# Kernel optimization log

Measured on AMD Instinct MI355X. Metric: run time of the kernel, lower is better.

## Reference

```python
import jax, jax.numpy as jnp
import numpy as np

NOISE_EPS = 1e-2   # Shazeer noisy-gating stddev floor
LN_EPS = 1e-6
LOSS_COEF = 0.01
K = 2              # num_activated_experts


def _layer_norm(x, w, b):
    mu = jnp.mean(x, axis=-1, keepdims=True)
    var = jnp.var(x, axis=-1, keepdims=True)
    return (x - mu) * jax.lax.rsqrt(var + LN_EPS) * w + b


def _cv_squared(v):
    return jnp.var(v) / (jnp.mean(v) ** 2 + 1e-10)


def _normal_cdf(z):
    return 0.5 * (1.0 + jax.scipy.special.erf(z / jnp.sqrt(jnp.asarray(2.0, z.dtype))))


def setup_inputs() -> dict:
    key = jax.random.key(0)
    ks = jax.random.split(key, 8)
    N, D, H, O, E = 8192, 512, 1024, 512, 8
    x = jax.random.normal(ks[0], (N, D), jnp.float32)
    x_offsets = jnp.sort(jax.random.randint(ks[1], (17,), 0, N)).astype(jnp.int64)
    noise = jax.random.normal(ks[2], (N, E), jnp.float32)
    s = 0.02
    return {
        "x": x,
        "x_offsets": x_offsets,
        "max_seq_len": 2048,
        "noise": noise,
        "norm_w": jnp.ones((D,), jnp.float32),
        "norm_bias": jnp.zeros((D,), jnp.float32),
        "w_gate": jax.random.normal(ks[3], (D, E), jnp.float32) * s,
        "w_noise": jax.random.normal(ks[4], (D, E), jnp.float32) * s,
        "W1": jax.random.normal(ks[5], (E, H, D), jnp.float32) * s,  # [E, model_d, input]
        "b1": jnp.zeros((E, H), jnp.float32),
        "W2": jax.random.normal(ks[6], (E, O, H), jnp.float32) * s,  # [E, output, model_d]
        "b2": jnp.zeros((E, O), jnp.float32),
        "output_weight": jax.random.normal(ks[7], (D, O), jnp.float32) * s,
    }


def reference(x, x_offsets, max_seq_len, noise, norm_w, norm_bias, w_gate, w_noise,
              W1, b1, W2, b2, output_weight):
    N, D = x.shape
    E = w_gate.shape[1]
    k_plus = min(K + 1, E)

    # pre-norm
    x_norm = _layer_norm(x, norm_w, norm_bias)

    # noisy top-k gating (training path)
    clean_logits = x_norm @ w_gate                      # [N, E]
    noise_stddev = jax.nn.softplus(x_norm @ w_noise) + NOISE_EPS
    noisy_logits = clean_logits + noise * noise_stddev

    top_logits, top_indices = jax.lax.top_k(noisy_logits, k_plus)   # [N, k+1]
    top_k_logits = top_logits[:, :K]
    top_k_indices = top_indices[:, :K]
    top_k_gates = jax.nn.softmax(top_k_logits, axis=-1)             # [N, K]

    rows = jnp.arange(N)[:, None]
    gates = jnp.zeros((N, E), top_k_gates.dtype).at[rows, top_k_indices].set(top_k_gates)

    # load = prob each expert is in top-k under the gating noise (Shazeer)
    flat = top_logits.reshape(-1)
    pos_in = jnp.arange(N) * k_plus + K
    thr_in = flat[pos_in][:, None]          # (k+1)-th value: threshold if already in
    thr_out = flat[pos_in - 1][:, None]     # k-th value: threshold if currently out
    is_in = noisy_logits > thr_in
    prob_in = _normal_cdf((clean_logits - thr_in) / noise_stddev)
    prob_out = _normal_cdf((clean_logits - thr_out) / noise_stddev)
    load_probs = jnp.where(is_in, prob_in, prob_out)                # [N, E]

    loss = LOSS_COEF * (_cv_squared(gates.sum(0)) + _cv_squared(load_probs.sum(0)))

    # dispatch stats: tokens per expert
    lengths = jnp.zeros((E,), jnp.float32).at[top_k_indices.reshape(-1)].add(1.0)
    load = lengths / lengths.sum()

    # grouped expert MLP (dense one-hot combine; gates are 0 for unrouted experts)
    h = jnp.einsum('nd,ehd->neh', x_norm, W1) + b1                  # [N, E, H]
    a = jax.nn.silu(h)
    y_e = jnp.einsum('neh,eoh->neo', a, W2) + b2                    # [N, E, O]
    y_moe = jnp.einsum('ne,neo->no', gates, y_e)                    # [N, O]

    # shared expert: addmm(y, shared_x=x, output_weight)
    y = y_moe + x @ output_weight
    return y, loss, load
```

## Files before the change

kernel.cpp:

```cpp
#include <hip/hip_runtime.h>
#include <math.h>

typedef unsigned short u16;
typedef unsigned int u32;

#define N_ROWS 8192
#define DDIM 512
#define HDIM 1024
#define ODIM 512
#define NEXP 8
#define MAXPAIRS (N_ROWS * 2)
#define MAXPOS (MAXPAIRS + NEXP * 128)
#define MAXTILES (MAXPOS / 128)

#define SM_CNT 0
#define SM_CUR 8
#define SM_AOFF 16
#define SM_GSUM 32
#define SM_LSUM 40
#define SM_WORDS 64

using short8 = __attribute__((ext_vector_type(8))) short;
using float4v = __attribute__((ext_vector_type(4))) float;

__device__ __forceinline__ u16 f2bf(float f) {
    union { float f; u32 u; } v; v.f = f;
    u32 u = v.u;
    return (u16)((u + 0x7fffu + ((u >> 16) & 1u)) >> 16);
}

__device__ __forceinline__ void async_copy16(u16* lds, const u16* g) {
    __builtin_amdgcn_global_load_lds(
        (const __attribute__((address_space(1))) void*)g,
        (__attribute__((address_space(3))) void*)lds, 16, 0, 0);
}

__global__ __launch_bounds__(512) void init1_kernel(int* small, float* zeropage) {
    int i = threadIdx.x;
    if (i < SM_WORDS) small[i] = 0;
    zeropage[i] = 0.f;
}

#define W1CONV_BLOCKS 4096
#define GATE_BLOCKS 512
#define OWT_BLOCKS 256
#define BUCKET_BLOCKS 68
#define W2CONV_BLOCKS 2048
__global__ __launch_bounds__(256) void combo_kernel(
    const float* __restrict__ x, const float* __restrict__ noise,
    const float* __restrict__ norm_w, const float* __restrict__ norm_b,
    const float* __restrict__ w_gate, const float* __restrict__ w_noise,
    const float* __restrict__ W1, const float* __restrict__ ow,
    const float* __restrict__ W2,
    u16* __restrict__ xnorm_bf, u16* __restrict__ x_bf,
    int* __restrict__ pair_expert, float* __restrict__ pair_gate,
    u16* __restrict__ W1b, u16* __restrict__ owT, u16* __restrict__ W2b,
    int* __restrict__ small, int* __restrict__ bucket_rows)
{
    __shared__ __align__(16) float sh[NEXP * DDIM * 2 + 64];
    int b = blockIdx.x, tid = threadIdx.x;

    if (b >= GATE_BLOCKS) {
        int cb = b - GATE_BLOCKS;
        if (cb < W1CONV_BLOCKS) {
            size_t i = (size_t)cb * 256 + tid;
            float4 v = ((const float4*)W1)[i];
            ushort4 o;
            o.x = f2bf(v.x); o.y = f2bf(v.y); o.z = f2bf(v.z); o.w = f2bf(v.w);
            ((ushort4*)W1b)[i] = o;
        } else if (cb < W1CONV_BLOCKS + OWT_BLOCKS) {
            float (*tile)[33] = (float(*)[33])sh;
            int t = cb - W1CONV_BLOCKS;
            int bx = (t & 15) * 32, by = (t >> 4) * 32;
            int tx = tid & 31, ty = tid >> 5;
            for (int r = ty; r < 32; r += 8) tile[r][tx] = ow[(size_t)(by + r) * ODIM + bx + tx];
            __syncthreads();
            for (int r = ty; r < 32; r += 8) owT[(size_t)(bx + r) * DDIM + by + tx] = f2bf(tile[tx][r]);
        } else if (cb < W1CONV_BLOCKS + OWT_BLOCKS + BUCKET_BLOCKS) {
            int i = (cb - W1CONV_BLOCKS - OWT_BLOCKS) * 256 + tid;
            if (i < MAXPOS) bucket_rows[i] = -1;
        } else {
            int j = cb - W1CONV_BLOCKS - OWT_BLOCKS - BUCKET_BLOCKS;
            size_t i = (size_t)j * 512 + tid;
#pragma unroll
            for (int t = 0; t < 2; t++, i += 256) {
                float4 v = ((const float4*)W2)[i];
                ushort4 o;
                o.x = f2bf(v.x); o.y = f2bf(v.y); o.z = f2bf(v.z); o.w = f2bf(v.w);
                ((ushort4*)W2b)[i] = o;
            }
        }
        return;
    }

    float* wgT = sh;
    float* wnT = sh + NEXP * DDIM;
    float* blk_g = sh + 2 * NEXP * DDIM;
    float* blk_l = blk_g + NEXP;
    int* blk_c = (int*)(blk_l + NEXP);
    float* smf = (float*)small;

    for (int i = tid; i < NEXP * DDIM; i += 256) {
        int d = i >> 3, e = i & 7;
        wgT[e * DDIM + d] = w_gate[i];
        wnT[e * DDIM + d] = w_noise[i];
    }
    if (tid < NEXP) { blk_g[tid] = 0.f; blk_l[tid] = 0.f; blk_c[tid] = 0; }
    __syncthreads();

    int wave = tid >> 6, lane = tid & 63;
    float nw[8], nb[8];
#pragma unroll
    for (int j = 0; j < 8; j++) { nw[j] = norm_w[j * 64 + lane]; nb[j] = norm_b[j * 64 + lane]; }

    for (int r = 0; r < 4; ++r) {
        int row = b * 16 + wave * 4 + r;
        const float* xr = x + (size_t)row * DDIM;
        float xv[8], s = 0.f, s2 = 0.f;
#pragma unroll
        for (int j = 0; j < 8; j++) { float v = xr[j * 64 + lane]; xv[j] = v; s += v; s2 += v * v; }
#pragma unroll
        for (int o = 32; o; o >>= 1) { s += __shfl_xor(s, o, 64); s2 += __shfl_xor(s2, o, 64); }
        float mu = s * (1.f / DDIM);
        float var = s2 * (1.f / DDIM) - mu * mu;
        float rstd = rsqrtf(var + 1e-6f);

        float acc[16];
#pragma unroll
        for (int e = 0; e < 16; e++) acc[e] = 0.f;
#pragma unroll
        for (int j = 0; j < 8; j++) {
            float v = (xv[j] - mu) * rstd * nw[j] + nb[j];
            int d = j * 64 + lane;
            xnorm_bf[(size_t)row * DDIM + d] = f2bf(v);
            x_bf[(size_t)row * DDIM + d] = f2bf(xv[j]);
#pragma unroll
            for (int e = 0; e < 8; e++) {
                acc[e] += v * wgT[e * DDIM + d];
                acc[8 + e] += v * wnT[e * DDIM + d];
            }
        }
#pragma unroll
        for (int e = 0; e < 16; e++)
#pragma unroll
            for (int o = 32; o; o >>= 1) acc[e] += __shfl_xor(acc[e], o, 64);

        float cl[8], sd[8], nz[8];
#pragma unroll
        for (int e = 0; e < 8; e++) {
            cl[e] = acc[e];
            float t = acc[8 + e];
            float sp = fmaxf(t, 0.f) + log1pf(expf(-fabsf(t)));
            sd[e] = sp + 0.01f;
            nz[e] = cl[e] + noise[(size_t)row * NEXP + e] * sd[e];
        }
        int idx[3]; float val[3]; u32 msk = 0;
#pragma unroll
        for (int t = 0; t < 3; t++) {
            float best = -INFINITY; int bi = 0;
#pragma unroll
            for (int e = 0; e < 8; e++)
                if (!((msk >> e) & 1) && nz[e] > best) { best = nz[e]; bi = e; }
            idx[t] = bi; val[t] = best; msk |= 1u << bi;
        }
        float e1 = expf(val[1] - val[0]);
        float g0 = 1.f / (1.f + e1), g1 = e1 / (1.f + e1);
        float thr_in = val[2], thr_out = val[1];

        if (lane == 0) {
            pair_expert[row * 2] = idx[0]; pair_gate[row * 2] = g0;
            pair_expert[row * 2 + 1] = idx[1]; pair_gate[row * 2 + 1] = g1;
            atomicAdd(&blk_g[idx[0]], g0); atomicAdd(&blk_g[idx[1]], g1);
            atomicAdd(&blk_c[idx[0]], 1); atomicAdd(&blk_c[idx[1]], 1);
#pragma unroll
            for (int e = 0; e < 8; e++) {
                float thr = (nz[e] > thr_in) ? thr_in : thr_out;
                float z = (cl[e] - thr) / sd[e];
                float p = 0.5f * (1.f + erff(z * 0.70710678118654752f));
                atomicAdd(&blk_l[e], p);
            }
        }
    }
    __syncthreads();
    if (tid < NEXP) {
        atomicAdd(smf + SM_GSUM + tid, blk_g[tid]);
        atomicAdd(smf + SM_LSUM + tid, blk_l[tid]);
        atomicAdd(&small[SM_CNT + tid], blk_c[tid]);
    }
}

__global__ __launch_bounds__(256) void scatter_kernel(
    const int* __restrict__ pair_expert, const float* __restrict__ pair_gate,
    int* __restrict__ small, int* __restrict__ bucket_rows, float* __restrict__ gate_by_pos,
    float* __restrict__ out_loss, float* __restrict__ out_load)
{
    __shared__ int aoff[NEXP + 1];
    __shared__ int blk_cnt[NEXP];
    __shared__ int blk_base[NEXP];
    int tid = threadIdx.x;
    if (tid == 0) {
        int acc = 0; aoff[0] = 0;
        for (int e = 0; e < NEXP; e++) { acc += (small[SM_CNT + e] + 127) & ~127; aoff[e + 1] = acc; }
    }
    if (tid < NEXP) blk_cnt[tid] = 0;
    __syncthreads();
    int p = blockIdx.x * 256 + tid;
    int e = pair_expert[p];
    int local = atomicAdd(&blk_cnt[e], 1);
    __syncthreads();
    if (tid < NEXP)
        blk_base[tid] = aoff[tid] + atomicAdd(&small[SM_CUR + tid], blk_cnt[tid]);
    if (blockIdx.x == 0 && tid < NEXP + 1) small[SM_AOFF + tid] = aoff[tid];
    __syncthreads();
    int pos = blk_base[e] + local;
    bucket_rows[pos] = p >> 1;
    gate_by_pos[pos] = pair_gate[p];

    if (blockIdx.x == 0 && tid == 0) {
        const float* gs = (const float*)small + SM_GSUM;
        const float* ls = (const float*)small + SM_LSUM;
        float cv[2];
        for (int t = 0; t < 2; t++) {
            const float* v = t ? ls : gs;
            float m = 0.f;
            for (int k = 0; k < NEXP; k++) m += v[k];
            m *= (1.f / NEXP);
            float var = 0.f;
            for (int k = 0; k < NEXP; k++) { float d = v[k] - m; var += d * d; }
            var *= (1.f / NEXP);
            cv[t] = var / (m * m + 1e-10f);
        }
        out_loss[0] = 0.01f * (cv[0] + cv[1]);
        int tot = 0;
        for (int k = 0; k < NEXP; k++) tot += small[SM_CNT + k];
        float inv = 1.f / (float)tot;
        for (int k = 0; k < NEXP; k++) out_load[k] = (float)small[SM_CNT + k] * inv;
    }
}

__global__ __launch_bounds__(256) void gemmA_kernel(
    const u16* __restrict__ xnorm, const u16* __restrict__ W1b,
    const u16* __restrict__ xbf, const u16* __restrict__ owT,
    const int* __restrict__ bucket_rows, const int* __restrict__ small,
    const float* __restrict__ b1, const u16* __restrict__ zeropage,
    u16* __restrict__ a_buf, float* __restrict__ y)
{
    constexpr int KD = 512;
    __shared__ __align__(16) u16 As[128 * 64];
    __shared__ __align__(16) u16 Bs[128 * 64];

    int tid = threadIdx.x;
    if (blockIdx.y >= 8) {
        int j = (blockIdx.y - 8) * 136 + blockIdx.x;
        if (j >= 256) return;
        int base = (j >> 2) * 128, bn = (j & 3) * 128;
        int wave = tid >> 6, lane = tid & 63;
        const int lrow = lane >> 2;
        const int kcol = (((lane & 3) ^ ((lane >> 3) & 3)) * 8);
        const int trow = wave * 32 + lrow;
        int wm = (wave & 1) * 64, wn = (wave >> 1) * 64;
        int fr = lane & 15, kq = lane >> 4;
        const int kg = ((kq ^ ((fr >> 1) & 3)) * 8);
        const u16* ga0 = xbf + (size_t)(base + trow) * KD + kcol;
        const u16* ga1 = xbf + (size_t)(base + trow + 16) * KD + kcol;
        const u16* gb0 = owT + (size_t)(bn + trow) * KD + kcol;
        const u16* gb1 = owT + (size_t)(bn + trow + 16) * KD + kcol;
        u16* As2 = (u16*)As; u16* Bs2 = (u16*)Bs;
        const int ofA0 = (wave * 32) * 32, ofA1 = (wave * 32 + 16) * 32;

        float4v acc[4][4];
#pragma unroll
        for (int i = 0; i < 4; i++)
#pragma unroll
            for (int jj = 0; jj < 4; jj++) acc[i][jj] = (float4v){0.f, 0.f, 0.f, 0.f};

        async_copy16(As2 + ofA0, ga0); async_copy16(As2 + ofA1, ga1);
        async_copy16(Bs2 + ofA0, gb0); async_copy16(Bs2 + ofA1, gb1);
        __syncthreads();
        int cur = 0;
        for (int t = 0; t < 16; ++t) {
            int nxt = cur ^ 1;
            if (t + 1 < 16) {
                int k1 = (t + 1) << 5;
                async_copy16(As2 + nxt * 4096 + ofA0, ga0 + k1);
                async_copy16(As2 + nxt * 4096 + ofA1, ga1 + k1);
                async_copy16(Bs2 + nxt * 4096 + ofA0, gb0 + k1);
                async_copy16(Bs2 + nxt * 4096 + ofA1, gb1 + k1);
            }
            short8 af[4], bf[4];
#pragma unroll
            for (int mt = 0; mt < 4; mt++) af[mt] = *(const short8*)&As2[cur * 4096 + (wm + mt * 16 + fr) * 32 + kg];
#pragma unroll
            for (int nt = 0; nt < 4; nt++) bf[nt] = *(const short8*)&Bs2[cur * 4096 + (wn + nt * 16 + fr) * 32 + kg];
#pragma unroll
            for (int mt = 0; mt < 4; mt++)
#pragma unroll
                for (int nt = 0; nt < 4; nt++)
                    acc[mt][nt] = __builtin_amdgcn_mfma_f32_16x16x32_bf16(af[mt], bf[nt], acc[mt][nt], 0, 0, 0);
            __syncthreads();
            cur = nxt;
        }
        int rbase = (lane >> 4) * 4, c16 = lane & 15;
#pragma unroll
        for (int mt = 0; mt < 4; mt++) {
            int gm = base + wm + mt * 16 + rbase;
#pragma unroll
            for (int nt = 0; nt < 4; nt++) {
                int gn = bn + wn + nt * 16 + c16;
#pragma unroll
                for (int r = 0; r < 4; r++)
                    y[(size_t)(gm + r) * ODIM + gn] = acc[mt][nt][r];
            }
        }
        return;
    }

    int base = blockIdx.x * 128;
    if (base >= small[SM_AOFF + 8]) return;
    int e = 0;
    while (e < 7 && base >= small[SM_AOFF + e + 1]) ++e;
    int bn = blockIdx.y * 128;
    const u16* Bsel = W1b + (size_t)e * HDIM * KD;

    int wave = tid >> 6, lane = tid & 63;
    int lr = lane >> 3;
    int lc = ((lane & 7) ^ lr) * 8;

    const u16* ga[4]; const u16* gb[4];
    u16* la[4]; u16* lb[4];
#pragma unroll
    for (int c = 0; c < 4; c++) {
        int tr = wave * 32 + c * 8;
        int r0 = bucket_rows[base + tr + lr];
        ga[c] = ((r0 < 0) ? zeropage : xnorm + (size_t)r0 * KD) + lc;
        gb[c] = Bsel + (size_t)(bn + tr + lr) * KD + lc;
        la[c] = &As[tr * 64];
        lb[c] = &Bs[tr * 64];
    }

    int wm = (wave & 1) * 64, wn = (wave >> 1) * 64;
    int fr = lane & 15, kq = lane >> 4, f7 = fr & 7;

    float4v acc[4][4];
#pragma unroll
    for (int i = 0; i < 4; i++)
#pragma unroll
        for (int j = 0; j < 4; j++) acc[i][j] = (float4v){0.f, 0.f, 0.f, 0.f};

    for (int k0 = 0; k0 < KD; k0 += 64) {
        __syncthreads();
#pragma unroll
        for (int c = 0; c < 4; c++) async_copy16(la[c], ga[c] + k0);
#pragma unroll
        for (int c = 0; c < 4; c++) async_copy16(lb[c], gb[c] + k0);
        __syncthreads();
        short8 af[4][2], bf[4][2];
#pragma unroll
        for (int mt = 0; mt < 4; mt++)
#pragma unroll
            for (int kh = 0; kh < 2; kh++)
                af[mt][kh] = *(const short8*)&As[(wm + mt * 16 + fr) * 64 + (((kq + 4 * kh) ^ f7) * 8)];
#pragma unroll
        for (int nt = 0; nt < 4; nt++)
#pragma unroll
            for (int kh = 0; kh < 2; kh++)
                bf[nt][kh] = *(const short8*)&Bs[(wn + nt * 16 + fr) * 64 + (((kq + 4 * kh) ^ f7) * 8)];
#pragma unroll
        for (int mt = 0; mt < 4; mt++)
#pragma unroll
            for (int nt = 0; nt < 4; nt++) {
                acc[mt][nt] = __builtin_amdgcn_mfma_f32_16x16x32_bf16(af[mt][0], bf[nt][0], acc[mt][nt], 0, 0, 0);
                acc[mt][nt] = __builtin_amdgcn_mfma_f32_16x16x32_bf16(af[mt][1], bf[nt][1], acc[mt][nt], 0, 0, 0);
            }
    }

    int rbase = (lane >> 4) * 4, c16 = lane & 15;
#pragma unroll
    for (int nt = 0; nt < 4; nt++) {
        int gn = bn + wn + nt * 16 + c16;
        float bv = b1[e * HDIM + gn];
#pragma unroll
        for (int mt = 0; mt < 4; mt++) {
            int gm = base + wm + mt * 16 + rbase;
#pragma unroll
            for (int r = 0; r < 4; r++) {
                float h = acc[mt][nt][r] + bv;
                float a = h * __builtin_amdgcn_rcpf(1.f + __expf(-h));
                a_buf[(size_t)(gm + r) * HDIM + gn] = f2bf(a);
            }
        }
    }
}

__global__ __launch_bounds__(512) void gemmB_kernel(
    const u16* __restrict__ a_buf, const u16* __restrict__ W2b,
    const int* __restrict__ bucket_rows, const int* __restrict__ small,
    const float* __restrict__ b2, const float* __restrict__ gate_by_pos,
    float* __restrict__ y)
{
    constexpr int KD = 1024;
    __shared__ __align__(16) u16 As[2][128 * 32];
    __shared__ __align__(16) u16 Bs[2][256 * 32];

    int tid = threadIdx.x;
    int wave = tid >> 6, lane = tid & 63;
    const int lrow = lane >> 2;
    const int kcol = (((lane & 3) ^ ((lane >> 3) & 3)) * 8);
    int wm = (wave >> 2) * 64, wn = (wave & 3) * 64;
    int fr = lane & 15, kq = lane >> 4;
    const int kg = ((kq ^ ((fr >> 1) & 3)) * 8);

    int base = blockIdx.x * 128;
    if (base >= small[SM_AOFF + 8]) return;
    int e = 0;
    while (e < 7 && base >= small[SM_AOFF + e + 1]) ++e;
    int bn = blockIdx.y * 256;

    const u16* ga0 = a_buf + (size_t)(base + wave * 16 + lrow) * KD + kcol;
    const u16* Bsel = W2b + (size_t)e * ODIM * KD;
    const u16* gb0 = Bsel + (size_t)(bn + wave * 32 + lrow) * KD + kcol;
    const u16* gb1 = Bsel + (size_t)(bn + wave * 32 + 16 + lrow) * KD + kcol;
    const int ofA = (wave * 16) * 32;
    const int ofB0 = (wave * 32) * 32;
    const int ofB1 = (wave * 32 + 16) * 32;

    float4v acc[4][4];
#pragma unroll
    for (int i = 0; i < 4; i++)
#pragma unroll
        for (int j = 0; j < 4; j++) acc[i][j] = (float4v){0.f, 0.f, 0.f, 0.f};

    constexpr int nk = KD >> 5;
    async_copy16(&As[0][ofA], ga0);
    async_copy16(&Bs[0][ofB0], gb0);
    async_copy16(&Bs[0][ofB1], gb1);
    __syncthreads();

    int cur = 0;
    for (int t = 0; t < nk; ++t) {
        int nxt = cur ^ 1;
        if (t + 1 < nk) {
            int k1 = (t + 1) << 5;
            async_copy16(&As[nxt][ofA], ga0 + k1);
            async_copy16(&Bs[nxt][ofB0], gb0 + k1);
            async_copy16(&Bs[nxt][ofB1], gb1 + k1);
        }
        short8 af[4], bf[4];
#pragma unroll
        for (int mt = 0; mt < 4; mt++) af[mt] = *(const short8*)&As[cur][(wm + mt * 16 + fr) * 32 + kg];
#pragma unroll
        for (int nt = 0; nt < 4; nt++) bf[nt] = *(const short8*)&Bs[cur][(wn + nt * 16 + fr) * 32 + kg];
#pragma unroll
        for (int mt = 0; mt < 4; mt++)
#pragma unroll
            for (int nt = 0; nt < 4; nt++)
                acc[mt][nt] = __builtin_amdgcn_mfma_f32_16x16x32_bf16(af[mt], bf[nt], acc[mt][nt], 0, 0, 0);
        __syncthreads();
        cur = nxt;
    }

    int rbase = (lane >> 4) * 4, c16 = lane & 15;
#pragma unroll
    for (int mt = 0; mt < 4; mt++) {
        int pos0 = base + wm + mt * 16 + rbase;
        int rows[4]; float gs[4];
#pragma unroll
        for (int r = 0; r < 4; r++) { rows[r] = bucket_rows[pos0 + r]; gs[r] = gate_by_pos[pos0 + r]; }
#pragma unroll
        for (int nt = 0; nt < 4; nt++) {
            int gn = bn + wn + nt * 16 + c16;
            float b2v = b2[e * ODIM + gn];
#pragma unroll
            for (int r = 0; r < 4; r++) {
                if (rows[r] >= 0)
                    unsafeAtomicAdd(&y[(size_t)rows[r] * ODIM + gn], gs[r] * (acc[mt][nt][r] + b2v));
            }
        }
    }
}

extern "C" void kernel_launch(void* const* d_in, const int* in_sizes, int n_in,
                              void* d_out, int out_size, void* d_ws, size_t ws_size,
                              hipStream_t stream)
{
    (void)in_sizes; (void)n_in; (void)out_size; (void)ws_size;
    const float* x = (const float*)d_in[0];
    const float* noise = (const float*)d_in[3];
    const float* norm_w = (const float*)d_in[4];
    const float* norm_b = (const float*)d_in[5];
    const float* w_gate = (const float*)d_in[6];
    const float* w_noise = (const float*)d_in[7];
    const float* W1 = (const float*)d_in[8];
    const float* b1 = (const float*)d_in[9];
    const float* W2 = (const float*)d_in[10];
    const float* b2 = (const float*)d_in[11];
    const float* ow = (const float*)d_in[12];

    float* y = (float*)d_out;
    float* out_loss = y + (size_t)N_ROWS * ODIM;
    float* out_load = out_loss + 1;

    char* ws = (char*)d_ws;
    size_t off = 0;
    auto alloc = [&](size_t b) { size_t p = off; off = (off + b + 255) & ~(size_t)255; return p; };
    u16* xnorm_bf = (u16*)(ws + alloc((size_t)N_ROWS * DDIM * 2));
    u16* x_bf     = (u16*)(ws + alloc((size_t)N_ROWS * DDIM * 2));
    u16* W1b      = (u16*)(ws + alloc((size_t)NEXP * HDIM * DDIM * 2));
    u16* W2b      = (u16*)(ws + alloc((size_t)NEXP * ODIM * HDIM * 2));
    u16* owT      = (u16*)(ws + alloc((size_t)DDIM * ODIM * 2));
    u16* a_buf    = (u16*)(ws + alloc((size_t)MAXPOS * HDIM * 2));
    int* pair_expert = (int*)(ws + alloc((size_t)MAXPAIRS * 4));
    float* pair_gate = (float*)(ws + alloc((size_t)MAXPAIRS * 4));
    float* gate_by_pos = (float*)(ws + alloc((size_t)MAXPOS * 4));
    int* bucket_rows = (int*)(ws + alloc((size_t)MAXPOS * 4));
    int* small       = (int*)(ws + alloc(SM_WORDS * 4));
    float* zeropage  = (float*)(ws + alloc(2048));

    init1_kernel<<<1, 512, 0, stream>>>(small, zeropage);
    combo_kernel<<<GATE_BLOCKS + W1CONV_BLOCKS + OWT_BLOCKS + BUCKET_BLOCKS + W2CONV_BLOCKS,
                   256, 0, stream>>>(
        x, noise, norm_w, norm_b, w_gate, w_noise, W1, ow, W2,
        xnorm_bf, x_bf, pair_expert, pair_gate, W1b, owT, W2b, small, bucket_rows);
    scatter_kernel<<<MAXPAIRS / 256, 256, 0, stream>>>(pair_expert, pair_gate, small,
                                                       bucket_rows, gate_by_pos, out_loss, out_load);
    gemmA_kernel<<<dim3(MAXTILES, 8 + 2), 256, 0, stream>>>(xnorm_bf, W1b,
                                                            x_bf, owT, bucket_rows, small, b1,
                                                            (const u16*)zeropage, a_buf, y);
    gemmB_kernel<<<dim3(MAXTILES, 2), 512, 0, stream>>>(a_buf, W2b, bucket_rows,
                                                        small, b2, gate_by_pos, y);
}
```

Before: 250.8 us.

## Replace atomic scatter-add in expert GEMM epilogue with buffered combine kernel

The second expert GEMM now writes gated per-position outputs to a dense fp32 buffer instead of atomically adding into y. A new combine kernel reads each token's two routed positions, found through a row-to-position map recorded during scatter, and adds them to the shared-expert result in y. This is meant to remove contended float atomics to global memory, at the cost of an extra kernel launch and roughly 34 MB of extra fp32 writes and reads.

```diff
diff --git a/kernel.cpp b/kernel.cpp
--- a/kernel.cpp
+++ b/kernel.cpp
@@ -192,6 +192,7 @@
 __global__ __launch_bounds__(256) void scatter_kernel(
     const int* __restrict__ pair_expert, const float* __restrict__ pair_gate,
     int* __restrict__ small, int* __restrict__ bucket_rows, float* __restrict__ gate_by_pos,
+    int* __restrict__ rowpos,
     float* __restrict__ out_loss, float* __restrict__ out_load)
 {
     __shared__ int aoff[NEXP + 1];
@@ -215,6 +216,7 @@
     int pos = blk_base[e] + local;
     bucket_rows[pos] = p >> 1;
     gate_by_pos[pos] = pair_gate[p];
+    rowpos[p] = pos;
 
     if (blockIdx.x == 0 && tid == 0) {
         const float* gs = (const float*)small + SM_GSUM;
@@ -396,7 +398,7 @@
     const u16* __restrict__ a_buf, const u16* __restrict__ W2b,
     const int* __restrict__ bucket_rows, const int* __restrict__ small,
     const float* __restrict__ b2, const float* __restrict__ gate_by_pos,
-    float* __restrict__ y)
+    float* __restrict__ ye)
 {
     constexpr int KD = 1024;
     __shared__ __align__(16) u16 As[2][128 * 32];
@@ -473,9 +475,29 @@
 #pragma unroll
             for (int r = 0; r < 4; r++) {
                 if (rows[r] >= 0)
-                    unsafeAtomicAdd(&y[(size_t)rows[r] * ODIM + gn], gs[r] * (acc[mt][nt][r] + b2v));
-            }
-        }
+                    ye[(size_t)(pos0 + r) * ODIM + gn] = gs[r] * (acc[mt][nt][r] + b2v);
+            }
+        }
+    }
+}
+
+__global__ __launch_bounds__(256) void combine_kernel(
+    const float* __restrict__ ye, const int* __restrict__ rowpos,
+    float* __restrict__ y)
+{
+    int tid = threadIdx.x;
+    int row = blockIdx.x * 16 + (tid >> 4);
+    int c0 = (tid & 15) * 32;
+    int p0 = rowpos[row * 2];
+    int p1 = rowpos[row * 2 + 1];
+    const float4* e0 = (const float4*)(ye + (size_t)p0 * ODIM + c0);
+    const float4* e1 = (const float4*)(ye + (size_t)p1 * ODIM + c0);
+    float4* yp = (float4*)(y + (size_t)row * ODIM + c0);
+#pragma unroll
+    for (int i = 0; i < 8; i++) {
+        float4 a = yp[i], b = e0[i], c = e1[i];
+        a.x += b.x + c.x; a.y += b.y + c.y; a.z += b.z + c.z; a.w += b.w + c.w;
+        yp[i] = a;
     }
 }
 
@@ -509,10 +531,12 @@
     u16* W2b      = (u16*)(ws + alloc((size_t)NEXP * ODIM * HDIM * 2));
     u16* owT      = (u16*)(ws + alloc((size_t)DDIM * ODIM * 2));
     u16* a_buf    = (u16*)(ws + alloc((size_t)MAXPOS * HDIM * 2));
+    float* ye     = (float*)(ws + alloc((size_t)MAXPOS * ODIM * 4));
     int* pair_expert = (int*)(ws + alloc((size_t)MAXPAIRS * 4));
     float* pair_gate = (float*)(ws + alloc((size_t)MAXPAIRS * 4));
     float* gate_by_pos = (float*)(ws + alloc((size_t)MAXPOS * 4));
     int* bucket_rows = (int*)(ws + alloc((size_t)MAXPOS * 4));
+    int* rowpos      = (int*)(ws + alloc((size_t)MAXPAIRS * 4));
     int* small       = (int*)(ws + alloc(SM_WORDS * 4));
     float* zeropage  = (float*)(ws + alloc(2048));
 
@@ -522,10 +546,12 @@
         x, noise, norm_w, norm_b, w_gate, w_noise, W1, ow, W2,
         xnorm_bf, x_bf, pair_expert, pair_gate, W1b, owT, W2b, small, bucket_rows);
     scatter_kernel<<<MAXPAIRS / 256, 256, 0, stream>>>(pair_expert, pair_gate, small,
-                                                       bucket_rows, gate_by_pos, out_loss, out_load);
+                                                       bucket_rows, gate_by_pos, rowpos,
+                                                       out_loss, out_load);
     gemmA_kernel<<<dim3(MAXTILES, 8 + 2), 256, 0, stream>>>(xnorm_bf, W1b,
                                                             x_bf, owT, bucket_rows, small, b1,
                                                             (const u16*)zeropage, a_buf, y);
     gemmB_kernel<<<dim3(MAXTILES, 2), 512, 0, stream>>>(a_buf, W2b, bucket_rows,
-                                                        small, b2, gate_by_pos, y);
-}
+                                                        small, b2, gate_by_pos, ye);
+    combine_kernel<<<N_ROWS / 16, 256, 0, stream>>>(ye, rowpos, y);
+}
```

After: 248.0 us. About the same (-1.1%).

## Replace atomic scatter-add combine with per-position expert outputs gathered in shared-expert GEMM

Applied to the files above, without the earlier changes.

gemmB now writes gated expert outputs into a per-position fp32 buffer instead of atomically adding into y. A new gemmC kernel computes the shared-expert x@output_weight product and adds the two routed expert contributions, which it looks up through a row-to-position map that the scatter kernel now records. The shared GEMM moves out of gemmA, and gemmA/gemmB blocks are remapped so that consecutive blocks spread across the 8 column tiles. This removes atomic contention and the ordering dependency on y, in exchange for an extra kernel launch and roughly 35MB of fp32 intermediate written and then read back.

```diff
diff --git a/kernel.cpp b/kernel.cpp
--- a/kernel.cpp
+++ b/kernel.cpp
@@ -192,6 +192,7 @@
 __global__ __launch_bounds__(256) void scatter_kernel(
     const int* __restrict__ pair_expert, const float* __restrict__ pair_gate,
     int* __restrict__ small, int* __restrict__ bucket_rows, float* __restrict__ gate_by_pos,
+    int* __restrict__ rowpos,
     float* __restrict__ out_loss, float* __restrict__ out_load)
 {
     __shared__ int aoff[NEXP + 1];
@@ -215,6 +216,7 @@
     int pos = blk_base[e] + local;
     bucket_rows[pos] = p >> 1;
     gate_by_pos[pos] = pair_gate[p];
+    rowpos[p] = pos;
 
     if (blockIdx.x == 0 && tid == 0) {
         const float* gs = (const float*)small + SM_GSUM;
@@ -240,86 +242,22 @@
 
 __global__ __launch_bounds__(256) void gemmA_kernel(
     const u16* __restrict__ xnorm, const u16* __restrict__ W1b,
-    const u16* __restrict__ xbf, const u16* __restrict__ owT,
     const int* __restrict__ bucket_rows, const int* __restrict__ small,
     const float* __restrict__ b1, const u16* __restrict__ zeropage,
-    u16* __restrict__ a_buf, float* __restrict__ y)
+    u16* __restrict__ a_buf)
 {
     constexpr int KD = 512;
     __shared__ __align__(16) u16 As[128 * 64];
     __shared__ __align__(16) u16 Bs[128 * 64];
 
     int tid = threadIdx.x;
-    if (blockIdx.y >= 8) {
-        int j = (blockIdx.y - 8) * 136 + blockIdx.x;
-        if (j >= 256) return;
-        int base = (j >> 2) * 128, bn = (j & 3) * 128;
-        int wave = tid >> 6, lane = tid & 63;
-        const int lrow = lane >> 2;
-        const int kcol = (((lane & 3) ^ ((lane >> 3) & 3)) * 8);
-        const int trow = wave * 32 + lrow;
-        int wm = (wave & 1) * 64, wn = (wave >> 1) * 64;
-        int fr = lane & 15, kq = lane >> 4;
-        const int kg = ((kq ^ ((fr >> 1) & 3)) * 8);
-        const u16* ga0 = xbf + (size_t)(base + trow) * KD + kcol;
-        const u16* ga1 = xbf + (size_t)(base + trow + 16) * KD + kcol;
-        const u16* gb0 = owT + (size_t)(bn + trow) * KD + kcol;
-        const u16* gb1 = owT + (size_t)(bn + trow + 16) * KD + kcol;
-        u16* As2 = (u16*)As; u16* Bs2 = (u16*)Bs;
-        const int ofA0 = (wave * 32) * 32, ofA1 = (wave * 32 + 16) * 32;
-
-        float4v acc[4][4];
-#pragma unroll
-        for (int i = 0; i < 4; i++)
-#pragma unroll
-            for (int jj = 0; jj < 4; jj++) acc[i][jj] = (float4v){0.f, 0.f, 0.f, 0.f};
-
-        async_copy16(As2 + ofA0, ga0); async_copy16(As2 + ofA1, ga1);
-        async_copy16(Bs2 + ofA0, gb0); async_copy16(Bs2 + ofA1, gb1);
-        __syncthreads();
-        int cur = 0;
-        for (int t = 0; t < 16; ++t) {
-            int nxt = cur ^ 1;
-            if (t + 1 < 16) {
-                int k1 = (t + 1) << 5;
-                async_copy16(As2 + nxt * 4096 + ofA0, ga0 + k1);
-                async_copy16(As2 + nxt * 4096 + ofA1, ga1 + k1);
-                async_copy16(Bs2 + nxt * 4096 + ofA0, gb0 + k1);
-                async_copy16(Bs2 + nxt * 4096 + ofA1, gb1 + k1);
-            }
-            short8 af[4], bf[4];
-#pragma unroll
-            for (int mt = 0; mt < 4; mt++) af[mt] = *(const short8*)&As2[cur * 4096 + (wm + mt * 16 + fr) * 32 + kg];
-#pragma unroll
-            for (int nt = 0; nt < 4; nt++) bf[nt] = *(const short8*)&Bs2[cur * 4096 + (wn + nt * 16 + fr) * 32 + kg];
-#pragma unroll
-            for (int mt = 0; mt < 4; mt++)
-#pragma unroll
-                for (int nt = 0; nt < 4; nt++)
-                    acc[mt][nt] = __builtin_amdgcn_mfma_f32_16x16x32_bf16(af[mt], bf[nt], acc[mt][nt], 0, 0, 0);
-            __syncthreads();
-            cur = nxt;
-        }
-        int rbase = (lane >> 4) * 4, c16 = lane & 15;
-#pragma unroll
-        for (int mt = 0; mt < 4; mt++) {
-            int gm = base + wm + mt * 16 + rbase;
-#pragma unroll
-            for (int nt = 0; nt < 4; nt++) {
-                int gn = bn + wn + nt * 16 + c16;
-#pragma unroll
-                for (int r = 0; r < 4; r++)
-                    y[(size_t)(gm + r) * ODIM + gn] = acc[mt][nt][r];
-            }
-        }
-        return;
-    }
-
-    int base = blockIdx.x * 128;
+    int d = blockIdx.y * 136 + blockIdx.x;
+    int w = (d & 7) * 136 + (d >> 3);
+    int base = (w % 136) * 128;
+    int bn = (w / 136) * 128;
     if (base >= small[SM_AOFF + 8]) return;
     int e = 0;
     while (e < 7 && base >= small[SM_AOFF + e + 1]) ++e;
-    int bn = blockIdx.y * 128;
     const u16* Bsel = W1b + (size_t)e * HDIM * KD;
 
     int wave = tid >> 6, lane = tid & 63;
@@ -396,7 +334,7 @@
     const u16* __restrict__ a_buf, const u16* __restrict__ W2b,
     const int* __restrict__ bucket_rows, const int* __restrict__ small,
     const float* __restrict__ b2, const float* __restrict__ gate_by_pos,
-    float* __restrict__ y)
+    float* __restrict__ ye)
 {
     constexpr int KD = 1024;
     __shared__ __align__(16) u16 As[2][128 * 32];
@@ -410,11 +348,13 @@
     int fr = lane & 15, kq = lane >> 4;
     const int kg = ((kq ^ ((fr >> 1) & 3)) * 8);
 
-    int base = blockIdx.x * 128;
+    int d = blockIdx.y * 136 + blockIdx.x;
+    int w = (d & 7) * 34 + (d >> 3);
+    int base = (w % 136) * 128;
+    int bn = (w / 136) * 256;
     if (base >= small[SM_AOFF + 8]) return;
     int e = 0;
     while (e < 7 && base >= small[SM_AOFF + e + 1]) ++e;
-    int bn = blockIdx.y * 256;
 
     const u16* ga0 = a_buf + (size_t)(base + wave * 16 + lrow) * KD + kcol;
     const u16* Bsel = W2b + (size_t)e * ODIM * KD;
@@ -473,8 +413,87 @@
 #pragma unroll
             for (int r = 0; r < 4; r++) {
                 if (rows[r] >= 0)
-                    unsafeAtomicAdd(&y[(size_t)rows[r] * ODIM + gn], gs[r] * (acc[mt][nt][r] + b2v));
+                    ye[(size_t)(pos0 + r) * ODIM + gn] = gs[r] * (acc[mt][nt][r] + b2v);
             }
+        }
+    }
+}
+
+__global__ __launch_bounds__(256) void gemmC_kernel(
+    const u16* __restrict__ xbf, const u16* __restrict__ owT,
+    const int* __restrict__ rowpos, const float* __restrict__ ye,
+    float* __restrict__ y)
+{
+    constexpr int KD = 512;
+    __shared__ __align__(16) u16 As[2][128 * 32];
+    __shared__ __align__(16) u16 Bs[2][128 * 32];
+
+    int tid = threadIdx.x;
+    int d = blockIdx.y * 64 + blockIdx.x;
+    int w = (d & 7) * 32 + (d >> 3);
+    int base = (w & 63) * 128;
+    int bn = (w >> 6) * 128;
+
+    int wave = tid >> 6, lane = tid & 63;
+    const int lrow = lane >> 2;
+    const int kcol = (((lane & 3) ^ ((lane >> 3) & 3)) * 8);
+    const int trow = wave * 32 + lrow;
+    int wm = (wave & 1) * 64, wn = (wave >> 1) * 64;
+    int fr = lane & 15, kq = lane >> 4;
+    const int kg = ((kq ^ ((fr >> 1) & 3)) * 8);
+    const u16* ga0 = xbf + (size_t)(base + trow) * KD + kcol;
+    const u16* ga1 = xbf + (size_t)(base + trow + 16) * KD + kcol;
+    const u16* gb0 = owT + (size_t)(bn + trow) * KD + kcol;
+    const u16* gb1 = owT + (size_t)(bn + trow + 16) * KD + kcol;
+    const int ofA0 = (wave * 32) * 32, ofA1 = (wave * 32 + 16) * 32;
+
+    float4v acc[4][4];
+#pragma unroll
+    for (int i = 0; i < 4; i++)
+#pragma unroll
+        for (int j = 0; j < 4; j++) acc[i][j] = (float4v){0.f, 0.f, 0.f, 0.f};
+
+    async_copy16(&As[0][ofA0], ga0); async_copy16(&As[0][ofA1], ga1);
+    async_copy16(&Bs[0][ofA0], gb0); async_copy16(&Bs[0][ofA1], gb1);
+    __syncthreads();
+    int cur = 0;
+    for (int t = 0; t < 16; ++t) {
+        int nxt = cur ^ 1;
+        if (t + 1 < 16) {
+            int k1 = (t + 1) << 5;
+            async_copy16(&As[nxt][ofA0], ga0 + k1);
+            async_copy16(&As[nxt][ofA1], ga1 + k1);
+            async_copy16(&Bs[nxt][ofA0], gb0 + k1);
+            async_copy16(&Bs[nxt][ofA1], gb1 + k1);
+        }
+        short8 af[4], bf[4];
+#pragma unroll
+        for (int mt = 0; mt < 4; mt++) af[mt] = *(const short8*)&As[cur][(wm + mt * 16 + fr) * 32 + kg];
+#pragma unroll
+        for (int nt = 0; nt < 4; nt++) bf[nt] = *(const short8*)&Bs[cur][(wn + nt * 16 + fr) * 32 + kg];
+#pragma unroll
+        for (int mt = 0; mt < 4; mt++)
+#pragma unroll
+            for (int nt = 0; nt < 4; nt++)
+                acc[mt][nt] = __builtin_amdgcn_mfma_f32_16x16x32_bf16(af[mt], bf[nt], acc[mt][nt], 0, 0, 0);
+        __syncthreads();
+        cur = nxt;
+    }
+
+    int rbase = (lane >> 4) * 4, c16 = lane & 15;
+#pragma unroll
+    for (int mt = 0; mt < 4; mt++) {
+        int gm = base + wm + mt * 16 + rbase;
+        int p0[4], p1[4];
+#pragma unroll
+        for (int r = 0; r < 4; r++) { p0[r] = rowpos[(gm + r) * 2]; p1[r] = rowpos[(gm + r) * 2 + 1]; }
+#pragma unroll
+        for (int nt = 0; nt < 4; nt++) {
+            int gn = bn + wn + nt * 16 + c16;
+#pragma unroll
+            for (int r = 0; r < 4; r++)
+                y[(size_t)(gm + r) * ODIM + gn] = acc[mt][nt][r]
+                    + ye[(size_t)p0[r] * ODIM + gn] + ye[(size_t)p1[r] * ODIM + gn];
         }
     }
 }
@@ -509,10 +528,12 @@
     u16* W2b      = (u16*)(ws + alloc((size_t)NEXP * ODIM * HDIM * 2));
     u16* owT      = (u16*)(ws + alloc((size_t)DDIM * ODIM * 2));
     u16* a_buf    = (u16*)(ws + alloc((size_t)MAXPOS * HDIM * 2));
+    float* ye     = (float*)(ws + alloc((size_t)MAXPOS * ODIM * 4));
     int* pair_expert = (int*)(ws + alloc((size_t)MAXPAIRS * 4));
     float* pair_gate = (float*)(ws + alloc((size_t)MAXPAIRS * 4));
     float* gate_by_pos = (float*)(ws + alloc((size_t)MAXPOS * 4));
     int* bucket_rows = (int*)(ws + alloc((size_t)MAXPOS * 4));
+    int* rowpos      = (int*)(ws + alloc((size_t)MAXPAIRS * 4));
     int* small       = (int*)(ws + alloc(SM_WORDS * 4));
     float* zeropage  = (float*)(ws + alloc(2048));
 
@@ -522,10 +543,11 @@
         x, noise, norm_w, norm_b, w_gate, w_noise, W1, ow, W2,
         xnorm_bf, x_bf, pair_expert, pair_gate, W1b, owT, W2b, small, bucket_rows);
     scatter_kernel<<<MAXPAIRS / 256, 256, 0, stream>>>(pair_expert, pair_gate, small,
-                                                       bucket_rows, gate_by_pos, out_loss, out_load);
-    gemmA_kernel<<<dim3(MAXTILES, 8 + 2), 256, 0, stream>>>(xnorm_bf, W1b,
-                                                            x_bf, owT, bucket_rows, small, b1,
-                                                            (const u16*)zeropage, a_buf, y);
+                                                       bucket_rows, gate_by_pos, rowpos,
+                                                       out_loss, out_load);
+    gemmA_kernel<<<dim3(MAXTILES, 8), 256, 0, stream>>>(xnorm_bf, W1b, bucket_rows, small, b1,
+                                                        (const u16*)zeropage, a_buf);
     gemmB_kernel<<<dim3(MAXTILES, 2), 512, 0, stream>>>(a_buf, W2b, bucket_rows,
-                                                        small, b2, gate_by_pos, y);
-}
+                                                        small, b2, gate_by_pos, ye);
+    gemmC_kernel<<<dim3(64, 4), 256, 0, stream>>>(x_bf, owT, rowpos, ye, y);
+}
```

Result: slower. 261.9 us (+4.4%).
